# Performance work log

Hardware: AMD Instinct MI355X
Metric: run time of the kernel (lower is better)

The kernel has to match this reference:

```python
import jax, jax.numpy as jnp
import numpy as np

N = 50000   # nodes per graph stream
E = 800000  # edges per graph stream
G = 100     # graphs in batch
FIN, H = 74, 256


def setup_inputs() -> dict:
    key = jax.random.key(0)
    ks = jax.random.split(key, 16)
    d = {
        'xl': jax.random.normal(ks[0], (N, FIN), jnp.float32),
        'xr': jax.random.normal(ks[1], (N, FIN), jnp.float32),
        'src_l': jax.random.randint(ks[2], (E,), 0, N, jnp.int32),
        'dst_l': jax.random.randint(ks[3], (E,), 0, N, jnp.int32),
        'src_r': jax.random.randint(ks[4], (E,), 0, N, jnp.int32),
        'dst_r': jax.random.randint(ks[5], (E,), 0, N, jnp.int32),
        'gid_l': jnp.sort(jax.random.randint(ks[6], (N,), 0, G, jnp.int32)),
        'gid_r': jnp.sort(jax.random.randint(ks[7], (N,), 0, G, jnp.int32)),
        'W0': jax.random.normal(ks[8], (FIN, H), jnp.float32) / np.sqrt(FIN),
        'b0': jnp.zeros((H,), jnp.float32),
        'W1': jax.random.normal(ks[9], (H, H), jnp.float32) / np.sqrt(H),
        'b1': jnp.zeros((H,), jnp.float32),
        'W2': jax.random.normal(ks[10], (H, H), jnp.float32) / np.sqrt(H),
        'b2': jnp.zeros((H,), jnp.float32),
        'Wf1': jax.random.normal(ks[11], (2 * H, H), jnp.float32) / np.sqrt(2 * H),
        'bf1': jnp.zeros((H,), jnp.float32),
        'Wf2': jax.random.normal(ks[12], (H, 1), jnp.float32) / np.sqrt(H),
        'bf2': jnp.zeros((1,), jnp.float32),
    }
    return d


def _deg_isqrt(idx, n):
    deg = jax.ops.segment_sum(jnp.ones_like(idx, jnp.float32), idx, num_segments=n)
    return jax.lax.rsqrt(jnp.maximum(deg, 1.0))


def _graph_conv(x, src, dst, do_isq, di_isq, W, b):
    # DGL GraphConv, norm='both': h = relu(D_in^{-1/2} A D_out^{-1/2} X W + b)
    h = (x * do_isq[:, None]) @ W            # transform-first (in_feats >= out for layer0 path is fine mathematically)
    agg = jax.ops.segment_sum(h[src], dst, num_segments=x.shape[0])
    return jax.nn.relu(agg * di_isq[:, None] + b)


def reference(xl, xr, src_l, dst_l, src_r, dst_r, gid_l, gid_r,
              W0, b0, W1, b1, W2, b2, Wf1, bf1, Wf2, bf2):
    do_l, di_l = _deg_isqrt(src_l, N), _deg_isqrt(dst_l, N)
    do_r, di_r = _deg_isqrt(src_r, N), _deg_isqrt(dst_r, N)
    Ws, bs = (W0, W1, W2), (b0, b1, b2)
    hl, hr = xl, xr
    for W, b in zip(Ws, bs):  # shared weights across both graph streams
        hl = _graph_conv(hl, src_l, dst_l, do_l, di_l, W, b)
        hr = _graph_conv(hr, src_r, dst_r, do_r, di_r, W, b)
    pl = jax.ops.segment_sum(hl, gid_l, num_segments=G)  # dgl.sum_nodes
    pr = jax.ops.segment_sum(hr, gid_r, num_segments=G)
    z = jnp.concatenate([pl, pr], axis=-1)               # [G, 2H]
    return jax.nn.relu(z @ Wf1 + bf1) @ Wf2 + bf2        # [G, 1]
```

## Files before the change

### kernel.cpp

```cpp
#include <hip/hip_runtime.h>

#define N_NODES 50000
#define N_EDGES 800000
#define N_GRAPHS 100
#define FIN_DIM 74
#define K0 96
#define H_DIM 256
#define EG 3125
#define XS2_BLKS 9375
#define WCONV_BLKS 608
#define AGG0_BLKS 3128
#define AGGH_BLKS 6256
#define GEMM_BLKS 782
#define POOL_BLKS 782
#define SCAN_BLOCKS 196

typedef float f32x4 __attribute__((ext_vector_type(4)));
typedef float f32x2 __attribute__((ext_vector_type(2)));
typedef unsigned int u32x4 __attribute__((ext_vector_type(4)));
typedef unsigned short us2 __attribute__((ext_vector_type(2)));
typedef unsigned short us8 __attribute__((ext_vector_type(8)));
typedef __bf16 bf16x8 __attribute__((ext_vector_type(8)));

__device__ __forceinline__ unsigned short f2bf(float x) {
    unsigned u = __builtin_bit_cast(unsigned, x);
    u += 0x7fff + ((u >> 16) & 1);
    return (unsigned short)(u >> 16);
}
__device__ __forceinline__ float bf2f(unsigned short h) {
    return __builtin_bit_cast(float, (unsigned)h << 16);
}
__device__ __forceinline__ void acc8(float* a, us8 v) {
    u32x4 w = __builtin_bit_cast(u32x4, v);
    #pragma unroll
    for (int i = 0; i < 4; ++i) {
        a[2 * i]     += __builtin_bit_cast(float, w[i] << 16);
        a[2 * i + 1] += __builtin_bit_cast(float, w[i] & 0xffff0000u);
    }
}


__device__ __forceinline__ void hist_body(int bid, const int* __restrict__ src,
                                          const int* __restrict__ dst,
                                          int* __restrict__ cs, int* __restrict__ fc,
                                          int* __restrict__ rk) {
    int e = bid * 256 + threadIdx.x;
    if (e < N_EDGES) {
        rk[e] = atomicAdd(&fc[dst[e]], 1);
        atomicAdd(&cs[src[e]], 1);
    }
}

__device__ __forceinline__ void scat_body(int bid, const int* __restrict__ src,
                                          const int* __restrict__ dst,
                                          const int* __restrict__ rp,
                                          const int* __restrict__ rk,
                                          int* __restrict__ col) {
    int e = bid * 256 + threadIdx.x;
    if (e < N_EDGES) {
        int d = dst[e];
        col[rp[d] + rk[e]] = src[e];
    }
}

__device__ __forceinline__ void xscale_body(int bid, const float* __restrict__ x,
                                            const float* __restrict__ dso,
                                            unsigned short* __restrict__ xp) {
    int id = bid * 256 + threadIdx.x;
    int n = id / 48, f = (id - n * 48) * 2;
    float v0 = 0.f, v1 = 0.f;
    if (f < FIN_DIM) {
        f32x2 t = *(const f32x2*)&x[(size_t)n * FIN_DIM + f];
        float d = dso[n];
        v0 = t[0] * d; v1 = t[1] * d;
    }
    us2 r = { f2bf(v0), f2bf(v1) };
    *(us2*)&xp[(size_t)(f >> 4) * (N_NODES * 16) + (size_t)n * 16 + (f & 15)] = r;
}

__device__ __forceinline__ void wconv_body(int bid, const float* __restrict__ W0,
                                           const float* __restrict__ W1,
                                           const float* __restrict__ W2,
                                           unsigned short* __restrict__ Wt) {
    int id = bid * 256 + threadIdx.x;
    if (id < 256 * 96) {
        int n = id / 96, k = id - n * 96;
        float v = (k < FIN_DIM) ? W0[(size_t)k * H_DIM + n] : 0.f;
        Wt[id] = f2bf(v);
    } else if (id < 256 * 96 + 65536) {
        int id2 = id - 256 * 96;
        int n = id2 >> 8, k = id2 & 255;
        Wt[id] = f2bf(W1[(size_t)k * H_DIM + n]);
    } else {
        int id3 = id - 256 * 96 - 65536;
        int n = id3 >> 8, k = id3 & 255;
        Wt[id] = f2bf(W2[(size_t)k * H_DIM + n]);
    }
}

template<int SW, int NACT, int NSL>
__device__ __forceinline__ void agg_body(int abid, int cg,
                                         const unsigned short* __restrict__ h,
                                         const int* __restrict__ rp,
                                         const int* __restrict__ col,
                                         unsigned short* __restrict__ A) {
    const int CPB = SW / 8;
    const int NPB = 256 / CPB;
    if (cg >= NSL) return;
    int slot = threadIdx.x & (CPB - 1);
    int n = (abid >> 3) * NPB + threadIdx.x / CPB;
    if (n >= N_NODES) return;
    unsigned short* dst = A + (size_t)cg * (N_NODES * SW) + (size_t)n * SW + slot * 8;
    if (cg >= NACT) { us8 z = {}; *(us8*)dst = z; return; }
    const unsigned short* hs = h + (size_t)cg * (N_NODES * SW) + slot * 8;
    int beg = rp[n], end = rp[n + 1];
    float a[8] = {};
    int j = beg;
    for (; j + 3 < end; j += 4) {
        int s0 = col[j], s1 = col[j + 1], s2 = col[j + 2], s3 = col[j + 3];
        us8 v0 = *(const us8*)(hs + (size_t)s0 * SW);
        us8 v1 = *(const us8*)(hs + (size_t)s1 * SW);
        us8 v2 = *(const us8*)(hs + (size_t)s2 * SW);
        us8 v3 = *(const us8*)(hs + (size_t)s3 * SW);
        acc8(a, v0); acc8(a, v1); acc8(a, v2); acc8(a, v3);
    }
    for (; j < end; ++j)
        acc8(a, *(const us8*)(hs + (size_t)col[j] * SW));
    us8 r;
    #pragma unroll
    for (int i = 0; i < 8; ++i) r[i] = f2bf(a[i]);
    *(us8*)dst = r;
}

__device__ __forceinline__ void pool_body(int nb, const unsigned short* __restrict__ h,
                                          const int* __restrict__ gid,
                                          float* __restrict__ pool) {
    int n0 = nb * 64;
    int f = threadIdx.x;
    const unsigned short* hf = h + (size_t)(f >> 5) * (N_NODES * 32) + (f & 31);
    int end = min(n0 + 64, N_NODES);
    float acc = 0.0f;
    int gcur = gid[n0];
    for (int i = n0; i < end; ++i) {
        int g = gid[i];
        if (g != gcur) {
            atomicAdd(&pool[(size_t)gcur * H_DIM + f], acc);
            acc = 0.0f;
            gcur = g;
        }
        acc += bf2f(hf[(size_t)i * 32]);
    }
    atomicAdd(&pool[(size_t)gcur * H_DIM + f], acc);
}

template<int K, int SW>
__device__ __forceinline__ void gemm_body(int id, const unsigned short* __restrict__ A,
                                          const unsigned short* __restrict__ Wt,
                                          const float* __restrict__ bias,
                                          const float* __restrict__ dsi,
                                          const float* __restrict__ scale,
                                          unsigned short* __restrict__ C,
                                          unsigned short* smem) {
    unsigned short (*Ah)[40] = (unsigned short(*)[40])smem;
    unsigned short (*Bh)[40] = (unsigned short(*)[40])(smem + 128 * 40);
    const int M = N_NODES;

    int tid = threadIdx.x;
    int lane = tid & 63, wid = tid >> 6;
    int wm = (wid >> 1) * 64, wn = (wid & 1) * 64;
    int bm = (id >> 1) * 128, bn = (id & 1) * 128;

    f32x4 acc[4][4] = {};
    int r0 = wm + (lane & 15);
    int c0 = wn + (lane & 15);
    int kA = (lane >> 4) * 8;

    for (int k0 = 0; k0 < K; k0 += 32) {
        #pragma unroll
        for (int i = 0; i < 2; ++i) {
            int q = tid + i * 256;
            int row = q >> 2, k8 = (q & 3) * 8;
            int gm = bm + row;
            int kk = k0 + k8;
            us8 v = {};
            if (gm < M)
                v = *(const us8*)(A + (size_t)(kk / SW) * ((size_t)N_NODES * SW)
                                    + (size_t)gm * SW + (kk % SW));
            *(us8*)&Ah[row][k8] = v;
        }
        {
            int colx = tid & 127, kg = tid >> 7;
            const unsigned short* wsrc = Wt + (size_t)(bn + colx) * K + k0 + kg * 16;
            us8 w0 = *(const us8*)(wsrc);
            us8 w1 = *(const us8*)(wsrc + 8);
            *(us8*)&Bh[colx][kg * 16] = w0;
            *(us8*)&Bh[colx][kg * 16 + 8] = w1;
        }
        __syncthreads();

        bf16x8 ah[4], bh[4];
        #pragma unroll
        for (int m = 0; m < 4; ++m)
            ah[m] = __builtin_bit_cast(bf16x8, *(const us8*)&Ah[r0 + m * 16][kA]);
        #pragma unroll
        for (int n = 0; n < 4; ++n)
            bh[n] = __builtin_bit_cast(bf16x8, *(const us8*)&Bh[c0 + n * 16][kA]);

        #pragma unroll
        for (int m = 0; m < 4; ++m)
            #pragma unroll
            for (int n = 0; n < 4; ++n)
                acc[m][n] = __builtin_amdgcn_mfma_f32_16x16x32_bf16(ah[m], bh[n], acc[m][n], 0, 0, 0);
        __syncthreads();
    }

    int rowq = (lane >> 4) * 4;
    #pragma unroll
    for (int n = 0; n < 4; ++n) {
        int gn = bn + wn + n * 16 + (lane & 15);
        float bv = bias[gn];
        unsigned short* cs = C + (size_t)(gn >> 5) * (N_NODES * 32) + (gn & 31);
        #pragma unroll
        for (int m = 0; m < 4; ++m) {
            #pragma unroll
            for (int j = 0; j < 4; ++j) {
                int gm = bm + wm + m * 16 + rowq + j;
                if (gm < M) {
                    float r = fmaxf(acc[m][n][j] * dsi[gm] + bv, 0.0f);
                    if (scale) r *= scale[gm];
                    cs[(size_t)gm * 32] = f2bf(r);
                }
            }
        }
    }
}


__device__ __forceinline__ int block_excl_scan(int v, int* wsums) {
    int lane = threadIdx.x & 63, w = threadIdx.x >> 6;
    int x = v;
    #pragma unroll
    for (int ofs = 1; ofs < 64; ofs <<= 1) {
        int y = __shfl_up(x, ofs, 64);
        if (lane >= ofs) x += y;
    }
    if (lane == 63) wsums[w] = x;
    __syncthreads();
    int wo = 0;
    #pragma unroll
    for (int k = 0; k < 4; ++k) if (k < w) wo += wsums[k];
    return wo + x - v;
}

__global__ void k_hist2(const float* __restrict__ W0, const float* __restrict__ W1,
                        const float* __restrict__ W2, unsigned short* __restrict__ Wt,
                        const int* __restrict__ srcL, const int* __restrict__ dstL,
                        int* __restrict__ csL, int* __restrict__ fcL, int* __restrict__ rkL,
                        const int* __restrict__ srcR, const int* __restrict__ dstR,
                        int* __restrict__ csR, int* __restrict__ fcR, int* __restrict__ rkR) {
    int bid = blockIdx.x;
    if (bid < WCONV_BLKS)           wconv_body(bid, W0, W1, W2, Wt);
    else if (bid < WCONV_BLKS + EG) hist_body(bid - WCONV_BLKS, srcL, dstL, csL, fcL, rkL);
    else                            hist_body(bid - WCONV_BLKS - EG, srcR, dstR, csR, fcR, rkR);
}

__global__ void deg_scan1_kernel(const int* __restrict__ csL, const int* __restrict__ fcL,
                                 float* __restrict__ dsoL, float* __restrict__ dsiL,
                                 int* __restrict__ rpL, int* __restrict__ bsL,
                                 const int* __restrict__ csR, const int* __restrict__ fcR,
                                 float* __restrict__ dsoR, float* __restrict__ dsiR,
                                 int* __restrict__ rpR, int* __restrict__ bsR) {
    const int* cs = blockIdx.y ? csR : csL;
    const int* fc = blockIdx.y ? fcR : fcL;
    float* dso = blockIdx.y ? dsoR : dsoL;
    float* dsi = blockIdx.y ? dsiR : dsiL;
    int* rp = blockIdx.y ? rpR : rpL;
    int* bs = blockIdx.y ? bsR : bsL;
    __shared__ int ws[4];
    int i = blockIdx.x * 256 + threadIdx.x;
    int v = 0;
    if (i < N_NODES) {
        dso[i] = rsqrtf(fmaxf((float)cs[i], 1.0f));
        v = fc[i];
        dsi[i] = rsqrtf(fmaxf((float)v, 1.0f));
    }
    int ex = block_excl_scan(v, ws);
    if (i < N_NODES) rp[i] = ex;
    if (threadIdx.x == 255) bs[blockIdx.x] = ex + v;
}

__global__ void scan2_kernel(int* __restrict__ bsL, int* __restrict__ bsR, int nb) {
    int* bs = blockIdx.y ? bsR : bsL;
    __shared__ int ws[4];
    int i = threadIdx.x;
    int v = (i < nb) ? bs[i] : 0;
    int ex = block_excl_scan(v, ws);
    __syncthreads();
    if (i < nb) bs[i] = ex;
}

__global__ void scan3_kernel(int* __restrict__ rpL, const int* __restrict__ bsL,
                             int* __restrict__ rpR, const int* __restrict__ bsR) {
    int* rp = blockIdx.y ? rpR : rpL;
    const int* bs = blockIdx.y ? bsR : bsL;
    int i = blockIdx.x * 256 + threadIdx.x;
    if (i < N_NODES) rp[i] += bs[blockIdx.x];
    if (i == 0) rp[N_NODES] = N_EDGES;
}

__global__ void fuse_ssxx(const int* __restrict__ srcL, const int* __restrict__ dstL,
                          const int* __restrict__ rpL, const int* __restrict__ rkL,
                          int* __restrict__ colL,
                          const int* __restrict__ srcR, const int* __restrict__ dstR,
                          const int* __restrict__ rpR, const int* __restrict__ rkR,
                          int* __restrict__ colR,
                          const float* __restrict__ xL, const float* __restrict__ dsoL,
                          unsigned short* __restrict__ xpL,
                          const float* __restrict__ xR, const float* __restrict__ dsoR,
                          unsigned short* __restrict__ xpR) {
    int bid = blockIdx.x;
    if (bid < EG)                         scat_body(bid, srcL, dstL, rpL, rkL, colL);
    else if (bid < 2 * EG)                scat_body(bid - EG, srcR, dstR, rpR, rkR, colR);
    else if (bid < 2 * EG + XS2_BLKS)     xscale_body(bid - 2 * EG, xL, dsoL, xpL);
    else                                  xscale_body(bid - 2 * EG - XS2_BLKS, xR, dsoR, xpR);
}

__global__ void fuse_agg2_l0(const unsigned short* __restrict__ hL, const int* __restrict__ rpL,
                             const int* __restrict__ colL, unsigned short* __restrict__ AL,
                             const unsigned short* __restrict__ hR, const int* __restrict__ rpR,
                             const int* __restrict__ colR, unsigned short* __restrict__ AR) {
    int bid = blockIdx.x;
    if (bid < AGG0_BLKS) agg_body<16, 5, 6>(bid, bid & 7, hL, rpL, colL, AL);
    else {
        int lb = bid - AGG0_BLKS;
        agg_body<16, 5, 6>(lb, lb & 7, hR, rpR, colR, AR);
    }
}

template<int SOFF_L, int SOFF_R>
__global__ void fuse_agg2_half(const unsigned short* __restrict__ hL, const int* __restrict__ rpL,
                               const int* __restrict__ colL, unsigned short* __restrict__ AL,
                               const unsigned short* __restrict__ hR, const int* __restrict__ rpR,
                               const int* __restrict__ colR, unsigned short* __restrict__ AR) {
    int bid = blockIdx.x;
    int lane = bid & 7, grp = bid >> 3;
    if (lane < 4) agg_body<32, 8, 8>(grp << 3, SOFF_L + lane, hL, rpL, colL, AL);
    else          agg_body<32, 8, 8>(grp << 3, SOFF_R + (lane - 4), hR, rpR, colR, AR);
}

template<int K, int SW>
__global__ __launch_bounds__(256) void gemm_pair2(
        const unsigned short* __restrict__ AL, const float* __restrict__ dsiL,
        const float* __restrict__ scL, unsigned short* __restrict__ CL,
        const unsigned short* __restrict__ AR, const float* __restrict__ dsiR,
        const float* __restrict__ scR, unsigned short* __restrict__ CR,
        const unsigned short* __restrict__ Wt, const float* __restrict__ bias) {
    __shared__ unsigned short smem[2 * 128 * 40];
    int bid = blockIdx.x;
    if (bid < GEMM_BLKS) gemm_body<K, SW>(bid, AL, Wt, bias, dsiL, scL, CL, smem);
    else                 gemm_body<K, SW>(bid - GEMM_BLKS, AR, Wt, bias, dsiR, scR, CR, smem);
}

__global__ void pool2_kernel(const unsigned short* __restrict__ hL, const int* __restrict__ gidL,
                             float* __restrict__ poolL,
                             const unsigned short* __restrict__ hR, const int* __restrict__ gidR,
                             float* __restrict__ poolR) {
    int bid = blockIdx.x;
    if (bid < POOL_BLKS) pool_body(bid, hL, gidL, poolL);
    else                 pool_body(bid - POOL_BLKS, hR, gidR, poolR);
}

__global__ __launch_bounds__(256) void mlp_kernel(
        const float* __restrict__ pl, const float* __restrict__ pr,
        const float* __restrict__ Wf1, const float* __restrict__ bf1,
        const float* __restrict__ Wf2, const float* __restrict__ bf2,
        float* __restrict__ out) {
    __shared__ float z[512];
    __shared__ float red[256];
    int g = blockIdx.x, tid = threadIdx.x;
    z[tid] = pl[(size_t)g * H_DIM + tid];
    z[tid + 256] = pr[(size_t)g * H_DIM + tid];
    __syncthreads();
    float t = bf1[tid];
    #pragma unroll 8
    for (int k = 0; k < 512; ++k) t += z[k] * Wf1[(size_t)k * H_DIM + tid];
    t = fmaxf(t, 0.0f);
    red[tid] = t * Wf2[tid];
    __syncthreads();
    for (int ofs = 128; ofs > 0; ofs >>= 1) {
        if (tid < ofs) red[tid] += red[tid + ofs];
        __syncthreads();
    }
    if (tid == 0) out[g] = red[0] + bf2[0];
}


extern "C" void kernel_launch(void* const* d_in, const int* in_sizes, int n_in,
                              void* d_out, int out_size, void* d_ws, size_t ws_size,
                              hipStream_t stream) {
    const float* xl   = (const float*)d_in[0];
    const float* xr   = (const float*)d_in[1];
    const int* src_l  = (const int*)d_in[2];
    const int* dst_l  = (const int*)d_in[3];
    const int* src_r  = (const int*)d_in[4];
    const int* dst_r  = (const int*)d_in[5];
    const int* gid_l  = (const int*)d_in[6];
    const int* gid_r  = (const int*)d_in[7];
    const float* W0   = (const float*)d_in[8];
    const float* b0   = (const float*)d_in[9];
    const float* W1   = (const float*)d_in[10];
    const float* b1   = (const float*)d_in[11];
    const float* W2   = (const float*)d_in[12];
    const float* b2   = (const float*)d_in[13];
    const float* Wf1  = (const float*)d_in[14];
    const float* bf1  = (const float*)d_in[15];
    const float* Wf2  = (const float*)d_in[16];
    const float* bf2  = (const float*)d_in[17];
    float* out = (float*)d_out;
    (void)in_sizes; (void)n_in; (void)out_size; (void)ws_size;

    size_t off = 0;
    auto carve = [&](size_t bytes) {
        void* p = (char*)d_ws + off;
        off += (bytes + 255) & ~(size_t)255;
        return p;
    };
    const size_t NB4 = (size_t)N_NODES * 4;

    char* zstart = (char*)d_ws;
    int*   cs_l   = (int*)carve(NB4);
    int*   fc_l   = (int*)carve(NB4);
    int*   cs_r   = (int*)carve(NB4);
    int*   fc_r   = (int*)carve(NB4);
    float* pool_l = (float*)carve((size_t)N_GRAPHS * H_DIM * 4);
    float* pool_r = (float*)carve((size_t)N_GRAPHS * H_DIM * 4);
    size_t zbytes = off;

    float* dso_l = (float*)carve(NB4);
    float* dsi_l = (float*)carve(NB4);
    float* dso_r = (float*)carve(NB4);
    float* dsi_r = (float*)carve(NB4);
    int*   rp_l  = (int*)carve((size_t)(N_NODES + 1) * 4);
    int*   rp_r  = (int*)carve((size_t)(N_NODES + 1) * 4);
    int*   col_l = (int*)carve((size_t)N_EDGES * 4);
    int*   col_r = (int*)carve((size_t)N_EDGES * 4);
    int*   rk_l  = (int*)carve((size_t)N_EDGES * 4);
    int*   rk_r  = (int*)carve((size_t)N_EDGES * 4);
    int*   bs_l  = (int*)carve((size_t)SCAN_BLOCKS * 4);
    int*   bs_r  = (int*)carve((size_t)SCAN_BLOCKS * 4);

    unsigned short* Wt    = (unsigned short*)carve((size_t)(256 * 96 + 2 * 65536) * 2);
    unsigned short* Wt0   = Wt;
    unsigned short* Wt1   = Wt + 256 * 96;
    unsigned short* Wt2   = Wt + 256 * 96 + 65536;
    unsigned short* xp_l  = (unsigned short*)carve((size_t)N_NODES * 96 * 2);
    unsigned short* xp_r  = (unsigned short*)carve((size_t)N_NODES * 96 * 2);
    unsigned short* bufA_l = (unsigned short*)carve((size_t)N_NODES * H_DIM * 2);
    unsigned short* bufA_r = (unsigned short*)carve((size_t)N_NODES * H_DIM * 2);
    unsigned short* bufH_l = (unsigned short*)carve((size_t)N_NODES * H_DIM * 2);
    unsigned short* bufH_r = (unsigned short*)carve((size_t)N_NODES * H_DIM * 2);

    hipMemsetAsync(zstart, 0, zbytes, stream);

    k_hist2<<<WCONV_BLKS + 2 * EG, 256, 0, stream>>>(
        W0, W1, W2, Wt,
        src_l, dst_l, cs_l, fc_l, rk_l,
        src_r, dst_r, cs_r, fc_r, rk_r);

    deg_scan1_kernel<<<dim3(SCAN_BLOCKS, 2), 256, 0, stream>>>(
        cs_l, fc_l, dso_l, dsi_l, rp_l, bs_l,
        cs_r, fc_r, dso_r, dsi_r, rp_r, bs_r);
    scan2_kernel<<<dim3(1, 2), 256, 0, stream>>>(bs_l, bs_r, SCAN_BLOCKS);
    scan3_kernel<<<dim3(SCAN_BLOCKS, 2), 256, 0, stream>>>(rp_l, bs_l, rp_r, bs_r);

    fuse_ssxx<<<2 * EG + 2 * XS2_BLKS, 256, 0, stream>>>(
        src_l, dst_l, rp_l, rk_l, col_l,
        src_r, dst_r, rp_r, rk_r, col_r,
        xl, dso_l, xp_l,
        xr, dso_r, xp_r);

    fuse_agg2_l0<<<2 * AGG0_BLKS, 256, 0, stream>>>(
        xp_l, rp_l, col_l, bufA_l,
        xp_r, rp_r, col_r, bufA_r);
    gemm_pair2<K0, 16><<<2 * GEMM_BLKS, 256, 0, stream>>>(
        bufA_l, dsi_l, dso_l, bufH_l,
        bufA_r, dsi_r, dso_r, bufH_r,
        Wt0, b0);

    fuse_agg2_half<0, 4><<<AGGH_BLKS, 256, 0, stream>>>(
        bufH_l, rp_l, col_l, bufA_l,
        bufH_r, rp_r, col_r, bufA_r);
    fuse_agg2_half<4, 0><<<AGGH_BLKS, 256, 0, stream>>>(
        bufH_l, rp_l, col_l, bufA_l,
        bufH_r, rp_r, col_r, bufA_r);
    gemm_pair2<H_DIM, 32><<<2 * GEMM_BLKS, 256, 0, stream>>>(
        bufA_l, dsi_l, dso_l, bufH_l,
        bufA_r, dsi_r, dso_r, bufH_r,
        Wt1, b1);

    fuse_agg2_half<0, 4><<<AGGH_BLKS, 256, 0, stream>>>(
        bufH_l, rp_l, col_l, bufA_l,
        bufH_r, rp_r, col_r, bufA_r);
    fuse_agg2_half<4, 0><<<AGGH_BLKS, 256, 0, stream>>>(
        bufH_l, rp_l, col_l, bufA_l,
        bufH_r, rp_r, col_r, bufA_r);
    gemm_pair2<H_DIM, 32><<<2 * GEMM_BLKS, 256, 0, stream>>>(
        bufA_l, dsi_l, nullptr, bufH_l,
        bufA_r, dsi_r, nullptr, bufH_r,
        Wt2, b2);

    pool2_kernel<<<2 * POOL_BLKS, 256, 0, stream>>>(
        bufH_l, gid_l, pool_l,
        bufH_r, gid_r, pool_r);
    mlp_kernel<<<N_GRAPHS, 256, 0, stream>>>(pool_l, pool_r, Wf1, bf1, Wf2, bf2, out);
}
```

Before: 748.4 us.

## Move input bf16 conversion into histogram kernel, apply out-degree scale during aggregation

The layer-0 out-degree scaling moves out of the input conversion and into the aggregation gather, which now reads dso per source. The raw bf16 conversion of the inputs can then run in the first histogram kernel, so the scatter kernel shrinks to edge work only. Separately, the two half-width aggregation launches per hidden layer are merged into one launch, and the gather loop is unrolled by 8 for more loads in flight. This trades extra per-edge dso loads and multiplies for fewer launches and less serialized work after the scan.

```diff
diff --git a/kernel.cpp b/kernel.cpp
--- a/kernel.cpp
+++ b/kernel.cpp
@@ -7,7 +7,7 @@
 #define K0 96
 #define H_DIM 256
 #define EG 3125
-#define XS2_BLKS 9375
+#define XC_BLKS 9375
 #define WCONV_BLKS 608
 #define AGG0_BLKS 3128
 #define AGGH_BLKS 6256
@@ -36,6 +36,14 @@
     for (int i = 0; i < 4; ++i) {
         a[2 * i]     += __builtin_bit_cast(float, w[i] << 16);
         a[2 * i + 1] += __builtin_bit_cast(float, w[i] & 0xffff0000u);
+    }
+}
+__device__ __forceinline__ void acc8s(float* a, us8 v, float d) {
+    u32x4 w = __builtin_bit_cast(u32x4, v);
+    #pragma unroll
+    for (int i = 0; i < 4; ++i) {
+        a[2 * i]     += __builtin_bit_cast(float, w[i] << 16) * d;
+        a[2 * i + 1] += __builtin_bit_cast(float, w[i] & 0xffff0000u) * d;
     }
 }
 
@@ -63,16 +71,14 @@
     }
 }
 
-__device__ __forceinline__ void xscale_body(int bid, const float* __restrict__ x,
-                                            const float* __restrict__ dso,
-                                            unsigned short* __restrict__ xp) {
+__device__ __forceinline__ void xconv_body(int bid, const float* __restrict__ x,
+                                           unsigned short* __restrict__ xp) {
     int id = bid * 256 + threadIdx.x;
     int n = id / 48, f = (id - n * 48) * 2;
     float v0 = 0.f, v1 = 0.f;
     if (f < FIN_DIM) {
         f32x2 t = *(const f32x2*)&x[(size_t)n * FIN_DIM + f];
-        float d = dso[n];
-        v0 = t[0] * d; v1 = t[1] * d;
+        v0 = t[0]; v1 = t[1];
     }
     us2 r = { f2bf(v0), f2bf(v1) };
     *(us2*)&xp[(size_t)(f >> 4) * (N_NODES * 16) + (size_t)n * 16 + (f & 15)] = r;
@@ -98,9 +104,10 @@
     }
 }
 
-template<int SW, int NACT, int NSL>
+template<int SW, int NACT, int NSL, bool DSO>
 __device__ __forceinline__ void agg_body(int abid, int cg,
                                          const unsigned short* __restrict__ h,
+                                         const float* __restrict__ dso,
                                          const int* __restrict__ rp,
                                          const int* __restrict__ col,
                                          unsigned short* __restrict__ A) {
@@ -116,16 +123,45 @@
     int beg = rp[n], end = rp[n + 1];
     float a[8] = {};
     int j = beg;
+    for (; j + 7 < end; j += 8) {
+        int s[8];
+        #pragma unroll
+        for (int t = 0; t < 8; ++t) s[t] = col[j + t];
+        us8 v[8];
+        #pragma unroll
+        for (int t = 0; t < 8; ++t) v[t] = *(const us8*)(hs + (size_t)s[t] * SW);
+        if (DSO) {
+            float d[8];
+            #pragma unroll
+            for (int t = 0; t < 8; ++t) d[t] = dso[s[t]];
+            #pragma unroll
+            for (int t = 0; t < 8; ++t) acc8s(a, v[t], d[t]);
+        } else {
+            #pragma unroll
+            for (int t = 0; t < 8; ++t) acc8(a, v[t]);
+        }
+    }
     for (; j + 3 < end; j += 4) {
-        int s0 = col[j], s1 = col[j + 1], s2 = col[j + 2], s3 = col[j + 3];
-        us8 v0 = *(const us8*)(hs + (size_t)s0 * SW);
-        us8 v1 = *(const us8*)(hs + (size_t)s1 * SW);
-        us8 v2 = *(const us8*)(hs + (size_t)s2 * SW);
-        us8 v3 = *(const us8*)(hs + (size_t)s3 * SW);
-        acc8(a, v0); acc8(a, v1); acc8(a, v2); acc8(a, v3);
-    }
-    for (; j < end; ++j)
-        acc8(a, *(const us8*)(hs + (size_t)col[j] * SW));
+        int s[4];
+        #pragma unroll
+        for (int t = 0; t < 4; ++t) s[t] = col[j + t];
+        us8 v[4];
+        #pragma unroll
+        for (int t = 0; t < 4; ++t) v[t] = *(const us8*)(hs + (size_t)s[t] * SW);
+        if (DSO) {
+            #pragma unroll
+            for (int t = 0; t < 4; ++t) acc8s(a, v[t], dso[s[t]]);
+        } else {
+            #pragma unroll
+            for (int t = 0; t < 4; ++t) acc8(a, v[t]);
+        }
+    }
+    for (; j < end; ++j) {
+        int s = col[j];
+        us8 v = *(const us8*)(hs + (size_t)s * SW);
+        if (DSO) acc8s(a, v, dso[s]);
+        else     acc8(a, v);
+    }
     us8 r;
     #pragma unroll
     for (int i = 0; i < 8; ++i) r[i] = f2bf(a[i]);
@@ -252,16 +288,22 @@
     return wo + x - v;
 }
 
-__global__ void k_hist2(const float* __restrict__ W0, const float* __restrict__ W1,
-                        const float* __restrict__ W2, unsigned short* __restrict__ Wt,
-                        const int* __restrict__ srcL, const int* __restrict__ dstL,
+__global__ void k_hist2(const int* __restrict__ srcL, const int* __restrict__ dstL,
                         int* __restrict__ csL, int* __restrict__ fcL, int* __restrict__ rkL,
                         const int* __restrict__ srcR, const int* __restrict__ dstR,
-                        int* __restrict__ csR, int* __restrict__ fcR, int* __restrict__ rkR) {
+                        int* __restrict__ csR, int* __restrict__ fcR, int* __restrict__ rkR,
+                        const float* __restrict__ W0, const float* __restrict__ W1,
+                        const float* __restrict__ W2, unsigned short* __restrict__ Wt,
+                        const float* __restrict__ xL, unsigned short* __restrict__ xpL,
+                        const float* __restrict__ xR, unsigned short* __restrict__ xpR) {
     int bid = blockIdx.x;
-    if (bid < WCONV_BLKS)           wconv_body(bid, W0, W1, W2, Wt);
-    else if (bid < WCONV_BLKS + EG) hist_body(bid - WCONV_BLKS, srcL, dstL, csL, fcL, rkL);
-    else                            hist_body(bid - WCONV_BLKS - EG, srcR, dstR, csR, fcR, rkR);
+    if (bid < EG)                                hist_body(bid, srcL, dstL, csL, fcL, rkL);
+    else if (bid < 2 * EG)                       hist_body(bid - EG, srcR, dstR, csR, fcR, rkR);
+    else if (bid < 2 * EG + WCONV_BLKS)          wconv_body(bid - 2 * EG, W0, W1, W2, Wt);
+    else if (bid < 2 * EG + WCONV_BLKS + XC_BLKS)
+        xconv_body(bid - 2 * EG - WCONV_BLKS, xL, xpL);
+    else
+        xconv_body(bid - 2 * EG - WCONV_BLKS - XC_BLKS, xR, xpR);
 }
 
 __global__ void deg_scan1_kernel(const int* __restrict__ csL, const int* __restrict__ fcL,
@@ -308,44 +350,41 @@
     if (i == 0) rp[N_NODES] = N_EDGES;
 }
 
-__global__ void fuse_ssxx(const int* __restrict__ srcL, const int* __restrict__ dstL,
-                          const int* __restrict__ rpL, const int* __restrict__ rkL,
-                          int* __restrict__ colL,
-                          const int* __restrict__ srcR, const int* __restrict__ dstR,
-                          const int* __restrict__ rpR, const int* __restrict__ rkR,
-                          int* __restrict__ colR,
-                          const float* __restrict__ xL, const float* __restrict__ dsoL,
-                          unsigned short* __restrict__ xpL,
-                          const float* __restrict__ xR, const float* __restrict__ dsoR,
-                          unsigned short* __restrict__ xpR) {
+__global__ void k_scat2(const int* __restrict__ srcL, const int* __restrict__ dstL,
+                        const int* __restrict__ rpL, const int* __restrict__ rkL,
+                        int* __restrict__ colL,
+                        const int* __restrict__ srcR, const int* __restrict__ dstR,
+                        const int* __restrict__ rpR, const int* __restrict__ rkR,
+                        int* __restrict__ colR) {
     int bid = blockIdx.x;
-    if (bid < EG)                         scat_body(bid, srcL, dstL, rpL, rkL, colL);
-    else if (bid < 2 * EG)                scat_body(bid - EG, srcR, dstR, rpR, rkR, colR);
-    else if (bid < 2 * EG + XS2_BLKS)     xscale_body(bid - 2 * EG, xL, dsoL, xpL);
-    else                                  xscale_body(bid - 2 * EG - XS2_BLKS, xR, dsoR, xpR);
-}
-
-__global__ void fuse_agg2_l0(const unsigned short* __restrict__ hL, const int* __restrict__ rpL,
-                             const int* __restrict__ colL, unsigned short* __restrict__ AL,
-                             const unsigned short* __restrict__ hR, const int* __restrict__ rpR,
-                             const int* __restrict__ colR, unsigned short* __restrict__ AR) {
+    if (bid < EG) scat_body(bid, srcL, dstL, rpL, rkL, colL);
+    else          scat_body(bid - EG, srcR, dstR, rpR, rkR, colR);
+}
+
+__global__ void fuse_agg2_l0(const unsigned short* __restrict__ hL, const float* __restrict__ dsoL,
+                             const int* __restrict__ rpL, const int* __restrict__ colL,
+                             unsigned short* __restrict__ AL,
+                             const unsigned short* __restrict__ hR, const float* __restrict__ dsoR,
+                             const int* __restrict__ rpR, const int* __restrict__ colR,
+                             unsigned short* __restrict__ AR) {
     int bid = blockIdx.x;
-    if (bid < AGG0_BLKS) agg_body<16, 5, 6>(bid, bid & 7, hL, rpL, colL, AL);
+    if (bid < AGG0_BLKS) agg_body<16, 5, 6, true>(bid, bid & 7, hL, dsoL, rpL, colL, AL);
     else {
         int lb = bid - AGG0_BLKS;
-        agg_body<16, 5, 6>(lb, lb & 7, hR, rpR, colR, AR);
-    }
-}
-
-template<int SOFF_L, int SOFF_R>
-__global__ void fuse_agg2_half(const unsigned short* __restrict__ hL, const int* __restrict__ rpL,
-                               const int* __restrict__ colL, unsigned short* __restrict__ AL,
-                               const unsigned short* __restrict__ hR, const int* __restrict__ rpR,
-                               const int* __restrict__ colR, unsigned short* __restrict__ AR) {
+        agg_body<16, 5, 6, true>(lb, lb & 7, hR, dsoR, rpR, colR, AR);
+    }
+}
+
+__global__ void fuse_agg2_h(const unsigned short* __restrict__ hL, const int* __restrict__ rpL,
+                            const int* __restrict__ colL, unsigned short* __restrict__ AL,
+                            const unsigned short* __restrict__ hR, const int* __restrict__ rpR,
+                            const int* __restrict__ colR, unsigned short* __restrict__ AR) {
     int bid = blockIdx.x;
-    int lane = bid & 7, grp = bid >> 3;
-    if (lane < 4) agg_body<32, 8, 8>(grp << 3, SOFF_L + lane, hL, rpL, colL, AL);
-    else          agg_body<32, 8, 8>(grp << 3, SOFF_R + (lane - 4), hR, rpR, colR, AR);
+    if (bid < AGGH_BLKS) agg_body<32, 8, 8, false>(bid, bid & 7, hL, nullptr, rpL, colL, AL);
+    else {
+        int lb = bid - AGGH_BLKS;
+        agg_body<32, 8, 8, false>(lb, lb & 7, hR, nullptr, rpR, colR, AR);
+    }
 }
 
 template<int K, int SW>
@@ -462,10 +501,11 @@
 
     hipMemsetAsync(zstart, 0, zbytes, stream);
 
-    k_hist2<<<WCONV_BLKS + 2 * EG, 256, 0, stream>>>(
+    k_hist2<<<2 * EG + WCONV_BLKS + 2 * XC_BLKS, 256, 0, stream>>>(
+        src_l, dst_l, cs_l, fc_l, rk_l,
+        src_r, dst_r, cs_r, fc_r, rk_r,
         W0, W1, W2, Wt,
-        src_l, dst_l, cs_l, fc_l, rk_l,
-        src_r, dst_r, cs_r, fc_r, rk_r);
+        xl, xp_l, xr, xp_r);
 
     deg_scan1_kernel<<<dim3(SCAN_BLOCKS, 2), 256, 0, stream>>>(
         cs_l, fc_l, dso_l, dsi_l, rp_l, bs_l,
@@ -473,24 +513,19 @@
     scan2_kernel<<<dim3(1, 2), 256, 0, stream>>>(bs_l, bs_r, SCAN_BLOCKS);
     scan3_kernel<<<dim3(SCAN_BLOCKS, 2), 256, 0, stream>>>(rp_l, bs_l, rp_r, bs_r);
 
-    fuse_ssxx<<<2 * EG + 2 * XS2_BLKS, 256, 0, stream>>>(
+    k_scat2<<<2 * EG, 256, 0, stream>>>(
         src_l, dst_l, rp_l, rk_l, col_l,
-        src_r, dst_r, rp_r, rk_r, col_r,
-        xl, dso_l, xp_l,
-        xr, dso_r, xp_r);
+        src_r, dst_r, rp_r, rk_r, col_r);
 
     fuse_agg2_l0<<<2 * AGG0_BLKS, 256, 0, stream>>>(
-        xp_l, rp_l, col_l, bufA_l,
-        xp_r, rp_r, col_r, bufA_r);
+        xp_l, dso_l, rp_l, col_l, bufA_l,
+        xp_r, dso_r, rp_r, col_r, bufA_r);
     gemm_pair2<K0, 16><<<2 * GEMM_BLKS, 256, 0, stream>>>(
         bufA_l, dsi_l, dso_l, bufH_l,
         bufA_r, dsi_r, dso_r, bufH_r,
         Wt0, b0);
 
-    fuse_agg2_half<0, 4><<<AGGH_BLKS, 256, 0, stream>>>(
-        bufH_l, rp_l, col_l, bufA_l,
-        bufH_r, rp_r, col_r, bufA_r);
-    fuse_agg2_half<4, 0><<<AGGH_BLKS, 256, 0, stream>>>(
+    fuse_agg2_h<<<2 * AGGH_BLKS, 256, 0, stream>>>(
         bufH_l, rp_l, col_l, bufA_l,
         bufH_r, rp_r, col_r, bufA_r);
     gemm_pair2<H_DIM, 32><<<2 * GEMM_BLKS, 256, 0, stream>>>(
@@ -498,10 +533,7 @@
         bufA_r, dsi_r, dso_r, bufH_r,
         Wt1, b1);
 
-    fuse_agg2_half<0, 4><<<AGGH_BLKS, 256, 0, stream>>>(
-        bufH_l, rp_l, col_l, bufA_l,
-        bufH_r, rp_r, col_r, bufA_r);
-    fuse_agg2_half<4, 0><<<AGGH_BLKS, 256, 0, stream>>>(
+    fuse_agg2_h<<<2 * AGGH_BLKS, 256, 0, stream>>>(
         bufH_l, rp_l, col_l, bufA_l,
         bufH_r, rp_r, col_r, bufA_r);
     gemm_pair2<H_DIM, 32><<<2 * GEMM_BLKS, 256, 0, stream>>>(
```

After: 779.9 us. 4.2% more time.
